# Performance work log

Hardware: AMD Instinct MI355X
Metric: run time of the kernel (lower is better)

Reference implementation:

```python
import math
import jax, jax.numpy as jnp
import numpy as np

B, LQ, LK, D, DV = 16, 2048, 2048, 256, 256


def setup_inputs() -> dict:
    key = jax.random.key(0)
    k1, k2, k3, k4 = jax.random.split(key, 4)
    query = jax.random.normal(k1, (B, LQ, D), dtype=jnp.float32)
    kmat = jax.random.normal(k2, (B, LK, D), dtype=jnp.float32)
    value = jax.random.normal(k3, (B, LK, DV), dtype=jnp.float32)
    # per-batch valid lengths in [1, LK] (avoid 0 => all -inf row)
    valid_len = jax.random.randint(k4, (B,), 1, LK + 1, dtype=jnp.int64)
    return {"query": query, "key": kmat, "value": value, "valid_len": valid_len}


def reference(query, key, value, valid_len):
    d = query.shape[-1]
    # [B, Lq, Lk] scaled dot-product scores
    scores = jnp.einsum("bqd,bkd->bqk", query, key) / math.sqrt(d)
    # mask positions k >= valid_len[b] (same mask broadcast over all queries,
    # matching the repeat(1, Lq).view(shape) in the original masked_softmax)
    mask = jnp.arange(key.shape[1])[None, None, :] < valid_len[:, None, None]
    scores = jnp.where(mask, scores, -jnp.inf)
    attn = jax.nn.softmax(scores, axis=-1)  # dropout rate is 0.0 => identity
    return jnp.einsum("bqk,bkv->bqv", attn, value)
```

## Files before the change

kernel.cpp:

```cpp
#include <hip/hip_runtime.h>
#include <hip/hip_bf16.h>

#define B_   16
#define LQ_  2048
#define LK_  2048
#define D_   256
#define DV_  256
#define MINF -1.0e30f

typedef __bf16 bf16x8_t __attribute__((ext_vector_type(8)));
typedef short  s16x8    __attribute__((ext_vector_type(8)));
typedef short  s16x4    __attribute__((ext_vector_type(4)));
typedef float  f32x4    __attribute__((ext_vector_type(4)));

__device__ __forceinline__ unsigned short f2bf(float f) {
  unsigned int u = __builtin_bit_cast(unsigned int, f);
  u += 0x7fffu + ((u >> 16) & 1u);
  return (unsigned short)(u >> 16);
}

__device__ __forceinline__ s16x8 pack8(float4 a, float4 b) {
  s16x8 r;
  r[0] = (short)f2bf(a.x); r[1] = (short)f2bf(a.y);
  r[2] = (short)f2bf(a.z); r[3] = (short)f2bf(a.w);
  r[4] = (short)f2bf(b.x); r[5] = (short)f2bf(b.y);
  r[6] = (short)f2bf(b.z); r[7] = (short)f2bf(b.w);
  return r;
}

__device__ __forceinline__ void glds16(const unsigned short* g, unsigned short* l) {
  __builtin_amdgcn_global_load_lds(
      (const __attribute__((address_space(1))) unsigned int*)g,
      (__attribute__((address_space(3))) unsigned int*)l, 16, 0, 0);
}

__global__ __launch_bounds__(256) void prep_k(const float* __restrict__ K,
                                              unsigned short* __restrict__ wsK) {
  int gid = blockIdx.x * 256 + threadIdx.x;
  int gr = gid >> 5;
  int c  = gid & 31;
  const float* src = K + ((size_t)gr << 8) + c * 8;
  float4 a = *(const float4*)(src);
  float4 b = *(const float4*)(src + 4);
  *(s16x8*)(wsK + ((size_t)gr << 8) + ((c ^ (gr & 7)) << 3)) = pack8(a, b);
}

__global__ __launch_bounds__(256) void prep_v(const float* __restrict__ V,
                                              unsigned short* __restrict__ wsV) {
  __shared__ unsigned short t[256 * 72];
  const int tid = threadIdx.x;
  const float* src = V + (size_t)blockIdx.x * 64 * 256;
  #pragma unroll
  for (int i = 0; i < 16; ++i) {
    int idx = i * 256 + tid;
    int k   = idx >> 6;
    int dv0 = (idx & 63) * 4;
    float4 x = *(const float4*)(src + k * 256 + dv0);
    t[(dv0 + 0) * 72 + k] = f2bf(x.x);
    t[(dv0 + 1) * 72 + k] = f2bf(x.y);
    t[(dv0 + 2) * 72 + k] = f2bf(x.z);
    t[(dv0 + 3) * 72 + k] = f2bf(x.w);
  }
  __syncthreads();
  unsigned short* dst = wsV + (size_t)blockIdx.x * 16384;
  #pragma unroll
  for (int i = 0; i < 8; ++i) {
    int idx = i * 256 + tid;
    int dv = idx >> 3;
    int ch = idx & 7;
    s16x8 v = *(const s16x8*)(&t[dv * 72 + ch * 8]);
    *(s16x8*)(dst + dv * 64 + ((ch ^ (dv & 7)) << 3)) = v;
  }
}

__global__ __launch_bounds__(512, 2) void attn_fwd5(
    const float* __restrict__ Q, const unsigned short* __restrict__ wsK,
    const unsigned short* __restrict__ wsV, const int* __restrict__ VL,
    float* __restrict__ O) {
  __shared__ __align__(16) unsigned short lds_all[75776];

  const int tid  = threadIdx.x;
  const int wid  = tid >> 6;
  const int lane = tid & 63;
  const int l15  = lane & 15;
  const int lg   = lane >> 4;
  const int rq   = wid & 3;
  const int kh   = wid >> 2;

  const int bid = blockIdx.x;
  const int xcd = bid & 7;
  const int j   = bid >> 3;
  const int b   = xcd + ((j >> 4) << 3);
  const int qt  = j & 15;

  int n_k = (VL[1] == 0) ? VL[2 * b] : VL[b];
  if (n_k < 1) n_k = 1;
  if (n_k > LK_) n_k = LK_;
  const int nt = (n_k + 63) >> 6;

  const int qbase = qt * 128 + rq * 32;

  s16x8 qf[2][8];
  #pragma unroll
  for (int qc = 0; qc < 2; ++qc) {
    const float* qp = Q + ((size_t)b * LQ_ + qbase + qc * 16 + l15) * D_ + lg * 8;
    #pragma unroll
    for (int dk = 0; dk < 8; ++dk) {
      float4 a = *(const float4*)(qp + dk * 32);
      float4 c = *(const float4*)(qp + dk * 32 + 4);
      qf[qc][dk] = pack8(a, c);
    }
  }

  f32x4 o[2][16];
  #pragma unroll
  for (int qc = 0; qc < 2; ++qc)
    #pragma unroll
    for (int c = 0; c < 16; ++c) o[qc][c] = (f32x4){0.f, 0.f, 0.f, 0.f};
  float m[2] = {MINF, MINF}, l[2] = {0.f, 0.f};

  const unsigned short* kbw = wsK + (size_t)b * LK_ * D_;
  const unsigned short* vbw = wsV + (size_t)b * LK_ * DV_;
  unsigned short* pw = &lds_all[65536 + wid * 1280];

#define STAGE(buf, t) do {                                                    \
    const unsigned short* ks_ = kbw + (size_t)(t) * 16384;                    \
    const unsigned short* vs_ = vbw + (size_t)(t) * 16384;                    \
    _Pragma("unroll")                                                         \
    for (int p = 0; p < 4; ++p) {                                             \
      int cu = p * 512 + wid * 64;                                            \
      glds16(ks_ + (size_t)(cu + lane) * 8, &lds_all[(buf) * 16384 + cu * 8]);\
      glds16(vs_ + (size_t)(cu + lane) * 8,                                   \
             &lds_all[32768 + (buf) * 16384 + cu * 8]);                       \
    }                                                                         \
  } while (0)

  STAGE(0, 0);

  for (int t = 0; t < nt; ++t) {
    const int cur = t & 1;
    if (t + 1 < nt) {
      STAGE(cur ^ 1, t + 1);
      asm volatile("s_waitcnt vmcnt(8)" ::: "memory");
    } else {
      asm volatile("s_waitcnt vmcnt(0)" ::: "memory");
    }
    __builtin_amdgcn_s_barrier();
    __builtin_amdgcn_sched_barrier(0);

    const unsigned short* kl = &lds_all[cur * 16384];
    f32x4 s[2][2];
    __builtin_amdgcn_s_setprio(1);
    #pragma unroll
    for (int kc = 0; kc < 2; ++kc) {
      int krow = kh * 32 + kc * 16 + l15;
      int sw = (krow & 7) << 3;
      const unsigned short* base = kl + krow * 256;
      f32x4 a0 = (f32x4){0.f, 0.f, 0.f, 0.f};
      f32x4 a1 = (f32x4){0.f, 0.f, 0.f, 0.f};
      #pragma unroll
      for (int dk = 0; dk < 8; ++dk) {
        s16x8 kf = *(const s16x8*)(base + ((dk * 32 + lg * 8) ^ sw));
        a0 = __builtin_amdgcn_mfma_f32_16x16x32_bf16(
            __builtin_bit_cast(bf16x8_t, kf),
            __builtin_bit_cast(bf16x8_t, qf[0][dk]), a0, 0, 0, 0);
        a1 = __builtin_amdgcn_mfma_f32_16x16x32_bf16(
            __builtin_bit_cast(bf16x8_t, kf),
            __builtin_bit_cast(bf16x8_t, qf[1][dk]), a1, 0, 0, 0);
      }
      s[kc][0] = a0;
      s[kc][1] = a1;
    }
    __builtin_amdgcn_s_setprio(0);

    #pragma unroll
    for (int kc = 0; kc < 2; ++kc) {
      int gk = t * 64 + kh * 32 + kc * 16 + lg * 4;
      #pragma unroll
      for (int qc = 0; qc < 2; ++qc)
        #pragma unroll
        for (int j2 = 0; j2 < 4; ++j2)
          s[kc][qc][j2] = (gk + j2 < n_k) ? s[kc][qc][j2] * 0.0625f : MINF;
    }

    float pm[2];
    #pragma unroll
    for (int qc = 0; qc < 2; ++qc) {
      float v = fmaxf(fmaxf(s[0][qc][0], s[0][qc][1]),
                      fmaxf(s[0][qc][2], s[0][qc][3]));
      v = fmaxf(v, fmaxf(fmaxf(s[1][qc][0], s[1][qc][1]),
                         fmaxf(s[1][qc][2], s[1][qc][3])));
      v = fmaxf(v, __shfl_xor(v, 16, 64));
      v = fmaxf(v, __shfl_xor(v, 32, 64));
      pm[qc] = v;
    }
    if (__any((pm[0] > m[0] + 8.0f) || (pm[1] > m[1] + 8.0f))) {
      #pragma unroll
      for (int qc = 0; qc < 2; ++qc) {
        float mn = fmaxf(m[qc], pm[qc]);
        float sc = __expf(m[qc] - mn);
        m[qc] = mn; l[qc] *= sc;
        #pragma unroll
        for (int c = 0; c < 16; ++c) o[qc][c] = o[qc][c] * sc;
      }
    }
    #pragma unroll
    for (int qc = 0; qc < 2; ++qc) {
      float p[2][4];
      #pragma unroll
      for (int kc = 0; kc < 2; ++kc)
        #pragma unroll
        for (int j2 = 0; j2 < 4; ++j2)
          p[kc][j2] = __expf(s[kc][qc][j2] - m[qc]);
      float ps = ((p[0][0] + p[0][1]) + (p[0][2] + p[0][3]))
               + ((p[1][0] + p[1][1]) + (p[1][2] + p[1][3]));
      ps += __shfl_xor(ps, 16, 64);
      ps += __shfl_xor(ps, 32, 64);
      l[qc] += ps;
      #pragma unroll
      for (int kc = 0; kc < 2; ++kc) {
        s16x4 w;
        w[0] = (short)f2bf(p[kc][0]); w[1] = (short)f2bf(p[kc][1]);
        w[2] = (short)f2bf(p[kc][2]); w[3] = (short)f2bf(p[kc][3]);
        *(s16x4*)(pw + (qc * 16 + l15) * 40 + kc * 16 + lg * 4) = w;
      }
    }

    s16x8 pb[2];
    #pragma unroll
    for (int qc = 0; qc < 2; ++qc)
      pb[qc] = *(const s16x8*)(pw + (qc * 16 + l15) * 40 + lg * 8);

    const unsigned short* vl_ = &lds_all[32768 + cur * 16384];
    __builtin_amdgcn_s_setprio(1);
    #pragma unroll
    for (int c = 0; c < 16; ++c) {
      int dv = c * 16 + l15;
      s16x8 vf = *(const s16x8*)(vl_ + dv * 64 + (((kh * 4 + lg) ^ (dv & 7)) << 3));
      o[0][c] = __builtin_amdgcn_mfma_f32_16x16x32_bf16(
          __builtin_bit_cast(bf16x8_t, vf),
          __builtin_bit_cast(bf16x8_t, pb[0]), o[0][c], 0, 0, 0);
      o[1][c] = __builtin_amdgcn_mfma_f32_16x16x32_bf16(
          __builtin_bit_cast(bf16x8_t, vf),
          __builtin_bit_cast(bf16x8_t, pb[1]), o[1][c], 0, 0, 0);
    }
    __builtin_amdgcn_s_setprio(0);

    __builtin_amdgcn_sched_barrier(0);
    __builtin_amdgcn_s_barrier();
  }

  float* mo = (float*)lds_all + rq * 8448;
  if (kh == 1) {
    #pragma unroll
    for (int qc = 0; qc < 2; ++qc) {
      #pragma unroll
      for (int c = 0; c < 16; ++c)
        *(f32x4*)(mo + (qc * 16 + l15) * 260 + c * 16 + lg * 4) = o[qc][c];
      mo[8320 + qc * 16 + l15] = m[qc];
      mo[8352 + qc * 16 + l15] = l[qc];
    }
  }
  __syncthreads();
  if (kh == 0) {
    #pragma unroll
    for (int qc = 0; qc < 2; ++qc) {
      float mb = mo[8320 + qc * 16 + l15];
      float lb = mo[8352 + qc * 16 + l15];
      float M  = fmaxf(m[qc], mb);
      float sa = __expf(m[qc] - M), sb = __expf(mb - M);
      float invL = 1.0f / (sa * l[qc] + sb * lb);
      float* ob = O + ((size_t)b * LQ_ + qbase + qc * 16 + l15) * DV_;
      #pragma unroll
      for (int c = 0; c < 16; ++c) {
        int dvb = c * 16 + lg * 4;
        f32x4 mr = *(const f32x4*)(mo + (qc * 16 + l15) * 260 + dvb);
        f32x4 r;
        #pragma unroll
        for (int j2 = 0; j2 < 4; ++j2)
          r[j2] = (sa * o[qc][c][j2] + sb * mr[j2]) * invL;
        *(f32x4*)(ob + dvb) = r;
      }
    }
  }
#undef STAGE
}

__global__ __launch_bounds__(256) void attn_fwd(
    const float* __restrict__ Q, const float* __restrict__ K,
    const float* __restrict__ V, const int* __restrict__ VL,
    float* __restrict__ O) {
  __shared__ __align__(16) unsigned short lds_k[64 * D_];
  __shared__ __align__(16) unsigned short lds_v[DV_ * 64];
  __shared__ __align__(16) unsigned short lds_p[4][16 * 64];

  const int tid  = threadIdx.x;
  const int wid  = tid >> 6;
  const int lane = tid & 63;
  const int l15  = lane & 15;
  const int lg   = lane >> 4;
  const int bid = blockIdx.x;
  const int b   = bid >> 5;
  const int qt  = bid & 31;

  int n_k = (VL[1] == 0) ? VL[2 * b] : VL[b];
  if (n_k < 1) n_k = 1;
  if (n_k > LK_) n_k = LK_;

  const int qbase = qt * 64 + wid * 16;
  s16x8 qf[8];
  {
    const float* qp = Q + ((size_t)b * LQ_ + qbase + l15) * D_ + lg * 8;
    #pragma unroll
    for (int dk = 0; dk < 8; ++dk) {
      float4 a = *(const float4*)(qp + dk * 32);
      float4 c = *(const float4*)(qp + dk * 32 + 4);
      qf[dk] = pack8(a, c);
    }
  }
  f32x4 o[16];
  #pragma unroll
  for (int c = 0; c < 16; ++c) o[c] = (f32x4){0.f, 0.f, 0.f, 0.f};
  float m[4]    = {-INFINITY, -INFINITY, -INFINITY, -INFINITY};
  float lsum[4] = {0.f, 0.f, 0.f, 0.f};
  const float* kb = K + (size_t)b * LK_ * D_;
  const float* vb = V + (size_t)b * LK_ * DV_;
  const int nt = (n_k + 63) / 64;

  for (int kt = 0; kt < nt; ++kt) {
    __syncthreads();
    {
      const float* src = kb + (size_t)kt * 64 * D_;
      #pragma unroll
      for (int p = 0; p < 8; ++p) {
        int e = (p * 256 + tid) * 8;
        int r = e >> 8;
        int d = e & 255;
        float4 a = *(const float4*)(src + e);
        float4 c = *(const float4*)(src + e + 4);
        *(s16x8*)(&lds_k[r * 256 + (d ^ ((r & 7) << 3))]) = pack8(a, c);
      }
    }
    {
      const float* src = vb + (size_t)kt * 64 * DV_;
      #pragma unroll
      for (int p = 0; p < 2; ++p) {
        int item = p * 256 + tid;
        int k0  = (item >> 5) * 4;
        int dv0 = (item & 31) * 8;
        float va[4][8];
        #pragma unroll
        for (int r = 0; r < 4; ++r) {
          float4 x = *(const float4*)(src + (k0 + r) * DV_ + dv0);
          float4 y = *(const float4*)(src + (k0 + r) * DV_ + dv0 + 4);
          va[r][0]=x.x; va[r][1]=x.y; va[r][2]=x.z; va[r][3]=x.w;
          va[r][4]=y.x; va[r][5]=y.y; va[r][6]=y.z; va[r][7]=y.w;
        }
        #pragma unroll
        for (int i = 0; i < 8; ++i) {
          int dv = dv0 + i;
          s16x4 w;
          w[0]=(short)f2bf(va[0][i]); w[1]=(short)f2bf(va[1][i]);
          w[2]=(short)f2bf(va[2][i]); w[3]=(short)f2bf(va[3][i]);
          *(s16x4*)(&lds_v[dv * 64 + (k0 ^ ((dv & 7) << 3))]) = w;
        }
      }
    }
    __syncthreads();

    f32x4 s[4];
    #pragma unroll
    for (int kc = 0; kc < 4; ++kc) {
      f32x4 acc = (f32x4){0.f, 0.f, 0.f, 0.f};
      int krow = kc * 16 + l15;
      int sw = (krow & 7) << 3;
      #pragma unroll
      for (int dk = 0; dk < 8; ++dk) {
        s16x8 kf = *(const s16x8*)(&lds_k[krow * 256 + ((dk * 32 + lg * 8) ^ sw)]);
        acc = __builtin_amdgcn_mfma_f32_16x16x32_bf16(
            __builtin_bit_cast(bf16x8_t, qf[dk]),
            __builtin_bit_cast(bf16x8_t, kf), acc, 0, 0, 0);
      }
      s[kc] = acc;
    }
    #pragma unroll
    for (int kc = 0; kc < 4; ++kc) {
      int gk = kt * 64 + kc * 16 + l15;
      #pragma unroll
      for (int j = 0; j < 4; ++j) {
        float v = s[kc][j] * 0.0625f;
        s[kc][j] = (gk < n_k) ? v : -INFINITY;
      }
    }
    float pm[4];
    #pragma unroll
    for (int j = 0; j < 4; ++j)
      pm[j] = fmaxf(fmaxf(s[0][j], s[1][j]), fmaxf(s[2][j], s[3][j]));
    #pragma unroll
    for (int off = 1; off < 16; off <<= 1) {
      #pragma unroll
      for (int j = 0; j < 4; ++j)
        pm[j] = fmaxf(pm[j], __shfl_xor(pm[j], off, 64));
    }
    float sc[4];
    #pragma unroll
    for (int j = 0; j < 4; ++j) {
      float mn = fmaxf(m[j], pm[j]);
      sc[j] = __expf(m[j] - mn);
      m[j] = mn;
    }
    float psum[4] = {0.f, 0.f, 0.f, 0.f};
    #pragma unroll
    for (int kc = 0; kc < 4; ++kc) {
      #pragma unroll
      for (int j = 0; j < 4; ++j) {
        float p = __expf(s[kc][j] - m[j]);
        psum[j] += p;
        int r = lg * 4 + j;
        lds_p[wid][r * 64 + ((kc * 16 + l15) ^ ((r & 7) << 3))] = f2bf(p);
      }
    }
    #pragma unroll
    for (int off = 1; off < 16; off <<= 1) {
      #pragma unroll
      for (int j = 0; j < 4; ++j)
        psum[j] += __shfl_xor(psum[j], off, 64);
    }
    #pragma unroll
    for (int j = 0; j < 4; ++j) lsum[j] = lsum[j] * sc[j] + psum[j];
    #pragma unroll
    for (int c = 0; c < 16; ++c) {
      #pragma unroll
      for (int j = 0; j < 4; ++j) o[c][j] *= sc[j];
    }
    s16x8 pa[2];
    #pragma unroll
    for (int kk = 0; kk < 2; ++kk)
      pa[kk] = *(const s16x8*)(&lds_p[wid][l15 * 64 + ((kk * 32 + lg * 8) ^ ((l15 & 7) << 3))]);
    #pragma unroll
    for (int c = 0; c < 16; ++c) {
      #pragma unroll
      for (int kk = 0; kk < 2; ++kk) {
        int dv = c * 16 + l15;
        s16x8 vf = *(const s16x8*)(&lds_v[dv * 64 + ((kk * 32 + lg * 8) ^ ((dv & 7) << 3))]);
        o[c] = __builtin_amdgcn_mfma_f32_16x16x32_bf16(
            __builtin_bit_cast(bf16x8_t, pa[kk]),
            __builtin_bit_cast(bf16x8_t, vf), o[c], 0, 0, 0);
      }
    }
  }
  float inv[4];
  #pragma unroll
  for (int j = 0; j < 4; ++j) inv[j] = 1.0f / lsum[j];
  float* ob = O + ((size_t)b * LQ_ + qbase) * DV_;
  #pragma unroll
  for (int c = 0; c < 16; ++c) {
    #pragma unroll
    for (int j = 0; j < 4; ++j) {
      int r = lg * 4 + j;
      ob[(size_t)r * DV_ + c * 16 + l15] = o[c][j] * inv[j];
    }
  }
}

extern "C" void kernel_launch(void* const* d_in, const int* in_sizes, int n_in,
                              void* d_out, int out_size, void* d_ws, size_t ws_size,
                              hipStream_t stream) {
  const float* Q  = (const float*)d_in[0];
  const float* K  = (const float*)d_in[1];
  const float* V  = (const float*)d_in[2];
  const int*   VL = (const int*)d_in[3];
  float* O = (float*)d_out;

  const size_t kv_elems = (size_t)B_ * LK_ * D_;
  const size_t need = kv_elems * 2 * sizeof(unsigned short);
  if (ws_size >= need) {
    unsigned short* wsK = (unsigned short*)d_ws;
    unsigned short* wsV = wsK + kv_elems;
    prep_k<<<dim3(4096), dim3(256), 0, stream>>>(K, wsK);
    prep_v<<<dim3(512), dim3(256), 0, stream>>>(V, wsV);
    attn_fwd5<<<dim3(256), dim3(512), 0, stream>>>(Q, wsK, wsV, VL, O);
  } else {
    attn_fwd<<<dim3(512), dim3(256), 0, stream>>>(Q, K, V, VL, O);
  }
}
```

Before: 142.4 us.

## Balance variable-length attention work with sorted per-block schedule of paired tiles

Adds a scheduling kernel that sorts batches by valid length and gives each of 256 persistent blocks two 64-query tiles, one from a long batch and one from a short batch, so per-block work evens out. The attention kernel drops to 256 threads with 4 waves per tile and loops over its two assigned tiles. It also defers the cross-lane row-sum reduction to the end of the loop and only shuffles the max when a rescale is needed. The trade-offs are an extra tiny launch, lower per-CU occupancy, and a serial dependency between the two tiles in each block.

```diff
diff --git a/kernel.cpp b/kernel.cpp
--- a/kernel.cpp
+++ b/kernel.cpp
@@ -73,213 +73,249 @@
   }
 }
 
-__global__ __launch_bounds__(512, 2) void attn_fwd5(
+__global__ __launch_bounds__(256) void prep_sched(const int* __restrict__ VL,
+                                                  int* __restrict__ sched) {
+  __shared__ int ord[16];
+  if (threadIdx.x == 0) {
+    int nk[16], o[16];
+    const int wide = (VL[1] == 0);
+    for (int i = 0; i < 16; ++i) {
+      int v = wide ? VL[2 * i] : VL[i];
+      if (v < 1) v = 1;
+      if (v > LK_) v = LK_;
+      nk[i] = v; o[i] = i;
+    }
+    for (int i = 1; i < 16; ++i) {
+      int key = o[i], kv = nk[key], j = i - 1;
+      while (j >= 0 && nk[o[j]] < kv) { o[j + 1] = o[j]; --j; }
+      o[j + 1] = key;
+    }
+    for (int i = 0; i < 16; ++i) ord[i] = o[i];
+  }
+  __syncthreads();
+  for (int s = threadIdx.x; s < 512; s += 256) {
+    int w  = s & 255;
+    int un = s >> 8;
+    int i  = un ? (511 - w) : w;
+    int bsel = ord[i >> 5];
+    int qt   = i & 31;
+    sched[s] = bsel | (qt << 8);
+  }
+}
+
+__global__ __launch_bounds__(256, 1) void attn_fwd10(
     const float* __restrict__ Q, const unsigned short* __restrict__ wsK,
     const unsigned short* __restrict__ wsV, const int* __restrict__ VL,
-    float* __restrict__ O) {
-  __shared__ __align__(16) unsigned short lds_all[75776];
+    const int* __restrict__ sched, float* __restrict__ O) {
+  __shared__ __align__(16) unsigned short lds_all[70144];
 
   const int tid  = threadIdx.x;
   const int wid  = tid >> 6;
   const int lane = tid & 63;
   const int l15  = lane & 15;
   const int lg   = lane >> 4;
-  const int rq   = wid & 3;
-  const int kh   = wid >> 2;
-
-  const int bid = blockIdx.x;
-  const int xcd = bid & 7;
-  const int j   = bid >> 3;
-  const int b   = xcd + ((j >> 4) << 3);
-  const int qt  = j & 15;
-
-  int n_k = (VL[1] == 0) ? VL[2 * b] : VL[b];
-  if (n_k < 1) n_k = 1;
-  if (n_k > LK_) n_k = LK_;
-  const int nt = (n_k + 63) >> 6;
-
-  const int qbase = qt * 128 + rq * 32;
-
-  s16x8 qf[2][8];
-  #pragma unroll
-  for (int qc = 0; qc < 2; ++qc) {
-    const float* qp = Q + ((size_t)b * LQ_ + qbase + qc * 16 + l15) * D_ + lg * 8;
-    #pragma unroll
-    for (int dk = 0; dk < 8; ++dk) {
-      float4 a = *(const float4*)(qp + dk * 32);
-      float4 c = *(const float4*)(qp + dk * 32 + 4);
-      qf[qc][dk] = pack8(a, c);
-    }
-  }
-
-  f32x4 o[2][16];
-  #pragma unroll
-  for (int qc = 0; qc < 2; ++qc)
-    #pragma unroll
-    for (int c = 0; c < 16; ++c) o[qc][c] = (f32x4){0.f, 0.f, 0.f, 0.f};
-  float m[2] = {MINF, MINF}, l[2] = {0.f, 0.f};
-
-  const unsigned short* kbw = wsK + (size_t)b * LK_ * D_;
-  const unsigned short* vbw = wsV + (size_t)b * LK_ * DV_;
-  unsigned short* pw = &lds_all[65536 + wid * 1280];
+  const int rq   = wid & 1;
+  const int kh   = wid >> 1;
+
+  unsigned short* pw = &lds_all[65536 + wid * 1152];
 
 #define STAGE(buf, t) do {                                                    \
     const unsigned short* ks_ = kbw + (size_t)(t) * 16384;                    \
     const unsigned short* vs_ = vbw + (size_t)(t) * 16384;                    \
     _Pragma("unroll")                                                         \
-    for (int p = 0; p < 4; ++p) {                                             \
-      int cu = p * 512 + wid * 64;                                            \
+    for (int p = 0; p < 8; ++p) {                                             \
+      int cu = p * 256 + wid * 64;                                            \
       glds16(ks_ + (size_t)(cu + lane) * 8, &lds_all[(buf) * 16384 + cu * 8]);\
       glds16(vs_ + (size_t)(cu + lane) * 8,                                   \
              &lds_all[32768 + (buf) * 16384 + cu * 8]);                       \
     }                                                                         \
   } while (0)
 
-  STAGE(0, 0);
-
-  for (int t = 0; t < nt; ++t) {
-    const int cur = t & 1;
-    if (t + 1 < nt) {
-      STAGE(cur ^ 1, t + 1);
-      asm volatile("s_waitcnt vmcnt(8)" ::: "memory");
-    } else {
-      asm volatile("s_waitcnt vmcnt(0)" ::: "memory");
-    }
-    __builtin_amdgcn_s_barrier();
-    __builtin_amdgcn_sched_barrier(0);
-
-    const unsigned short* kl = &lds_all[cur * 16384];
-    f32x4 s[2][2];
-    __builtin_amdgcn_s_setprio(1);
-    #pragma unroll
-    for (int kc = 0; kc < 2; ++kc) {
-      int krow = kh * 32 + kc * 16 + l15;
-      int sw = (krow & 7) << 3;
-      const unsigned short* base = kl + krow * 256;
-      f32x4 a0 = (f32x4){0.f, 0.f, 0.f, 0.f};
-      f32x4 a1 = (f32x4){0.f, 0.f, 0.f, 0.f};
+  for (int un = 0; un < 2; ++un) {
+    const int e  = sched[blockIdx.x + un * 256];
+    const int b  = e & 255;
+    const int qt = e >> 8;
+
+    int n_k = (VL[1] == 0) ? VL[2 * b] : VL[b];
+    if (n_k < 1) n_k = 1;
+    if (n_k > LK_) n_k = LK_;
+    const int nt = (n_k + 63) >> 6;
+
+    const int qbase = qt * 64 + rq * 32;
+
+    s16x8 qf[2][8];
+    #pragma unroll
+    for (int qc = 0; qc < 2; ++qc) {
+      const float* qp = Q + ((size_t)b * LQ_ + qbase + qc * 16 + l15) * D_ + lg * 8;
       #pragma unroll
       for (int dk = 0; dk < 8; ++dk) {
-        s16x8 kf = *(const s16x8*)(base + ((dk * 32 + lg * 8) ^ sw));
-        a0 = __builtin_amdgcn_mfma_f32_16x16x32_bf16(
-            __builtin_bit_cast(bf16x8_t, kf),
-            __builtin_bit_cast(bf16x8_t, qf[0][dk]), a0, 0, 0, 0);
-        a1 = __builtin_amdgcn_mfma_f32_16x16x32_bf16(
-            __builtin_bit_cast(bf16x8_t, kf),
-            __builtin_bit_cast(bf16x8_t, qf[1][dk]), a1, 0, 0, 0);
-      }
-      s[kc][0] = a0;
-      s[kc][1] = a1;
-    }
-    __builtin_amdgcn_s_setprio(0);
-
-    #pragma unroll
-    for (int kc = 0; kc < 2; ++kc) {
-      int gk = t * 64 + kh * 32 + kc * 16 + lg * 4;
+        float4 a = *(const float4*)(qp + dk * 32);
+        float4 c = *(const float4*)(qp + dk * 32 + 4);
+        qf[qc][dk] = pack8(a, c);
+      }
+    }
+
+    f32x4 o[2][16];
+    #pragma unroll
+    for (int qc = 0; qc < 2; ++qc)
+      #pragma unroll
+      for (int c = 0; c < 16; ++c) o[qc][c] = (f32x4){0.f, 0.f, 0.f, 0.f};
+    float m[2] = {MINF, MINF}, l[2] = {0.f, 0.f};
+
+    const unsigned short* kbw = wsK + (size_t)b * LK_ * D_;
+    const unsigned short* vbw = wsV + (size_t)b * LK_ * DV_;
+
+    __syncthreads();
+    STAGE(0, 0);
+
+    for (int t = 0; t < nt; ++t) {
+      const int cur = t & 1;
+      if (t + 1 < nt) {
+        STAGE(cur ^ 1, t + 1);
+        asm volatile("s_waitcnt vmcnt(16)" ::: "memory");
+      } else {
+        asm volatile("s_waitcnt vmcnt(0)" ::: "memory");
+      }
+      __builtin_amdgcn_s_barrier();
+      __builtin_amdgcn_sched_barrier(0);
+
+      const unsigned short* kl = &lds_all[cur * 16384];
+      f32x4 s[2][2];
+      __builtin_amdgcn_s_setprio(1);
+      #pragma unroll
+      for (int kc = 0; kc < 2; ++kc) {
+        int krow = kh * 32 + kc * 16 + l15;
+        int sw = (krow & 7) << 3;
+        const unsigned short* kbase = kl + krow * 256;
+        f32x4 a0 = (f32x4){0.f, 0.f, 0.f, 0.f};
+        f32x4 a1 = (f32x4){0.f, 0.f, 0.f, 0.f};
+        #pragma unroll
+        for (int dk = 0; dk < 8; ++dk) {
+          s16x8 kf = *(const s16x8*)(kbase + ((dk * 32 + lg * 8) ^ sw));
+          a0 = __builtin_amdgcn_mfma_f32_16x16x32_bf16(
+              __builtin_bit_cast(bf16x8_t, kf),
+              __builtin_bit_cast(bf16x8_t, qf[0][dk]), a0, 0, 0, 0);
+          a1 = __builtin_amdgcn_mfma_f32_16x16x32_bf16(
+              __builtin_bit_cast(bf16x8_t, kf),
+              __builtin_bit_cast(bf16x8_t, qf[1][dk]), a1, 0, 0, 0);
+        }
+        s[kc][0] = a0;
+        s[kc][1] = a1;
+      }
+      __builtin_amdgcn_s_setprio(0);
+
+      #pragma unroll
+      for (int kc = 0; kc < 2; ++kc) {
+        int gk = t * 64 + kh * 32 + kc * 16 + lg * 4;
+        #pragma unroll
+        for (int qc = 0; qc < 2; ++qc)
+          #pragma unroll
+          for (int j2 = 0; j2 < 4; ++j2)
+            s[kc][qc][j2] = (gk + j2 < n_k) ? s[kc][qc][j2] * 0.0625f : MINF;
+      }
+
+      float pml[2];
+      #pragma unroll
+      for (int qc = 0; qc < 2; ++qc) {
+        float v = fmaxf(fmaxf(s[0][qc][0], s[0][qc][1]),
+                        fmaxf(s[0][qc][2], s[0][qc][3]));
+        v = fmaxf(v, fmaxf(fmaxf(s[1][qc][0], s[1][qc][1]),
+                           fmaxf(s[1][qc][2], s[1][qc][3])));
+        pml[qc] = v;
+      }
+      if (__any((pml[0] > m[0] + 8.0f) || (pml[1] > m[1] + 8.0f))) {
+        #pragma unroll
+        for (int qc = 0; qc < 2; ++qc) {
+          float pm = fmaxf(pml[qc], __shfl_xor(pml[qc], 16, 64));
+          pm = fmaxf(pm, __shfl_xor(pm, 32, 64));
+          float mn = fmaxf(m[qc], pm);
+          float sc = __expf(m[qc] - mn);
+          m[qc] = mn; l[qc] *= sc;
+          #pragma unroll
+          for (int c = 0; c < 16; ++c) o[qc][c] = o[qc][c] * sc;
+        }
+      }
+      #pragma unroll
+      for (int qc = 0; qc < 2; ++qc) {
+        float p[2][4];
+        #pragma unroll
+        for (int kc = 0; kc < 2; ++kc)
+          #pragma unroll
+          for (int j2 = 0; j2 < 4; ++j2)
+            p[kc][j2] = __expf(s[kc][qc][j2] - m[qc]);
+        l[qc] += ((p[0][0] + p[0][1]) + (p[0][2] + p[0][3]))
+               + ((p[1][0] + p[1][1]) + (p[1][2] + p[1][3]));
+        #pragma unroll
+        for (int kc = 0; kc < 2; ++kc) {
+          s16x4 w;
+          w[0] = (short)f2bf(p[kc][0]); w[1] = (short)f2bf(p[kc][1]);
+          w[2] = (short)f2bf(p[kc][2]); w[3] = (short)f2bf(p[kc][3]);
+          *(s16x4*)(pw + (qc * 16 + l15) * 36 + kc * 16 + lg * 4) = w;
+        }
+      }
+
+      s16x8 pb[2];
       #pragma unroll
       for (int qc = 0; qc < 2; ++qc)
-        #pragma unroll
-        for (int j2 = 0; j2 < 4; ++j2)
-          s[kc][qc][j2] = (gk + j2 < n_k) ? s[kc][qc][j2] * 0.0625f : MINF;
-    }
-
-    float pm[2];
+        pb[qc] = *(const s16x8*)(pw + (qc * 16 + l15) * 36 + lg * 8);
+
+      const unsigned short* vl_ = &lds_all[32768 + cur * 16384];
+      __builtin_amdgcn_s_setprio(1);
+      #pragma unroll
+      for (int c = 0; c < 16; ++c) {
+        int dv = c * 16 + l15;
+        s16x8 vf = *(const s16x8*)(vl_ + dv * 64 + (((kh * 4 + lg) ^ (dv & 7)) << 3));
+        o[0][c] = __builtin_amdgcn_mfma_f32_16x16x32_bf16(
+            __builtin_bit_cast(bf16x8_t, vf),
+            __builtin_bit_cast(bf16x8_t, pb[0]), o[0][c], 0, 0, 0);
+        o[1][c] = __builtin_amdgcn_mfma_f32_16x16x32_bf16(
+            __builtin_bit_cast(bf16x8_t, vf),
+            __builtin_bit_cast(bf16x8_t, pb[1]), o[1][c], 0, 0, 0);
+      }
+      __builtin_amdgcn_s_setprio(0);
+
+      __builtin_amdgcn_sched_barrier(0);
+      __builtin_amdgcn_s_barrier();
+    }
+
     #pragma unroll
     for (int qc = 0; qc < 2; ++qc) {
-      float v = fmaxf(fmaxf(s[0][qc][0], s[0][qc][1]),
-                      fmaxf(s[0][qc][2], s[0][qc][3]));
-      v = fmaxf(v, fmaxf(fmaxf(s[1][qc][0], s[1][qc][1]),
-                         fmaxf(s[1][qc][2], s[1][qc][3])));
-      v = fmaxf(v, __shfl_xor(v, 16, 64));
-      v = fmaxf(v, __shfl_xor(v, 32, 64));
-      pm[qc] = v;
-    }
-    if (__any((pm[0] > m[0] + 8.0f) || (pm[1] > m[1] + 8.0f))) {
+      l[qc] += __shfl_xor(l[qc], 16, 64);
+      l[qc] += __shfl_xor(l[qc], 32, 64);
+    }
+
+    __syncthreads();
+    float* mo = (float*)lds_all + rq * 8448;
+    if (kh == 1) {
       #pragma unroll
       for (int qc = 0; qc < 2; ++qc) {
-        float mn = fmaxf(m[qc], pm[qc]);
-        float sc = __expf(m[qc] - mn);
-        m[qc] = mn; l[qc] *= sc;
-        #pragma unroll
-        for (int c = 0; c < 16; ++c) o[qc][c] = o[qc][c] * sc;
-      }
-    }
-    #pragma unroll
-    for (int qc = 0; qc < 2; ++qc) {
-      float p[2][4];
-      #pragma unroll
-      for (int kc = 0; kc < 2; ++kc)
-        #pragma unroll
-        for (int j2 = 0; j2 < 4; ++j2)
-          p[kc][j2] = __expf(s[kc][qc][j2] - m[qc]);
-      float ps = ((p[0][0] + p[0][1]) + (p[0][2] + p[0][3]))
-               + ((p[1][0] + p[1][1]) + (p[1][2] + p[1][3]));
-      ps += __shfl_xor(ps, 16, 64);
-      ps += __shfl_xor(ps, 32, 64);
-      l[qc] += ps;
-      #pragma unroll
-      for (int kc = 0; kc < 2; ++kc) {
-        s16x4 w;
-        w[0] = (short)f2bf(p[kc][0]); w[1] = (short)f2bf(p[kc][1]);
-        w[2] = (short)f2bf(p[kc][2]); w[3] = (short)f2bf(p[kc][3]);
-        *(s16x4*)(pw + (qc * 16 + l15) * 40 + kc * 16 + lg * 4) = w;
-      }
-    }
-
-    s16x8 pb[2];
-    #pragma unroll
-    for (int qc = 0; qc < 2; ++qc)
-      pb[qc] = *(const s16x8*)(pw + (qc * 16 + l15) * 40 + lg * 8);
-
-    const unsigned short* vl_ = &lds_all[32768 + cur * 16384];
-    __builtin_amdgcn_s_setprio(1);
-    #pragma unroll
-    for (int c = 0; c < 16; ++c) {
-      int dv = c * 16 + l15;
-      s16x8 vf = *(const s16x8*)(vl_ + dv * 64 + (((kh * 4 + lg) ^ (dv & 7)) << 3));
-      o[0][c] = __builtin_amdgcn_mfma_f32_16x16x32_bf16(
-          __builtin_bit_cast(bf16x8_t, vf),
-          __builtin_bit_cast(bf16x8_t, pb[0]), o[0][c], 0, 0, 0);
-      o[1][c] = __builtin_amdgcn_mfma_f32_16x16x32_bf16(
-          __builtin_bit_cast(bf16x8_t, vf),
-          __builtin_bit_cast(bf16x8_t, pb[1]), o[1][c], 0, 0, 0);
-    }
-    __builtin_amdgcn_s_setprio(0);
-
-    __builtin_amdgcn_sched_barrier(0);
-    __builtin_amdgcn_s_barrier();
-  }
-
-  float* mo = (float*)lds_all + rq * 8448;
-  if (kh == 1) {
-    #pragma unroll
-    for (int qc = 0; qc < 2; ++qc) {
-      #pragma unroll
-      for (int c = 0; c < 16; ++c)
-        *(f32x4*)(mo + (qc * 16 + l15) * 260 + c * 16 + lg * 4) = o[qc][c];
-      mo[8320 + qc * 16 + l15] = m[qc];
-      mo[8352 + qc * 16 + l15] = l[qc];
-    }
-  }
-  __syncthreads();
-  if (kh == 0) {
-    #pragma unroll
-    for (int qc = 0; qc < 2; ++qc) {
-      float mb = mo[8320 + qc * 16 + l15];
-      float lb = mo[8352 + qc * 16 + l15];
-      float M  = fmaxf(m[qc], mb);
-      float sa = __expf(m[qc] - M), sb = __expf(mb - M);
-      float invL = 1.0f / (sa * l[qc] + sb * lb);
-      float* ob = O + ((size_t)b * LQ_ + qbase + qc * 16 + l15) * DV_;
-      #pragma unroll
-      for (int c = 0; c < 16; ++c) {
-        int dvb = c * 16 + lg * 4;
-        f32x4 mr = *(const f32x4*)(mo + (qc * 16 + l15) * 260 + dvb);
-        f32x4 r;
-        #pragma unroll
-        for (int j2 = 0; j2 < 4; ++j2)
-          r[j2] = (sa * o[qc][c][j2] + sb * mr[j2]) * invL;
-        *(f32x4*)(ob + dvb) = r;
+        #pragma unroll
+        for (int c = 0; c < 16; ++c)
+          *(f32x4*)(mo + (qc * 16 + l15) * 260 + c * 16 + lg * 4) = o[qc][c];
+        mo[8320 + qc * 16 + l15] = m[qc];
+        mo[8352 + qc * 16 + l15] = l[qc];
+      }
+    }
+    __syncthreads();
+    if (kh == 0) {
+      #pragma unroll
+      for (int qc = 0; qc < 2; ++qc) {
+        float mb = mo[8320 + qc * 16 + l15];
+        float lb = mo[8352 + qc * 16 + l15];
+        float M  = fmaxf(m[qc], mb);
+        float sa = __expf(m[qc] - M), sb = __expf(mb - M);
+        float invL = 1.0f / (sa * l[qc] + sb * lb);
+        float* ob = O + ((size_t)b * LQ_ + qbase + qc * 16 + l15) * DV_;
+        #pragma unroll
+        for (int c = 0; c < 16; ++c) {
+          int dvb = c * 16 + lg * 4;
+          f32x4 mr = *(const f32x4*)(mo + (qc * 16 + l15) * 260 + dvb);
+          f32x4 r;
+          #pragma unroll
+          for (int j2 = 0; j2 < 4; ++j2)
+            r[j2] = (sa * o[qc][c][j2] + sb * mr[j2]) * invL;
+          *(f32x4*)(ob + dvb) = r;
+        }
       }
     }
   }
@@ -416,8 +452,8 @@
       for (int j = 0; j < 4; ++j) {
         float p = __expf(s[kc][j] - m[j]);
         psum[j] += p;
-        int r = lg * 4 + j;
-        lds_p[wid][r * 64 + ((kc * 16 + l15) ^ ((r & 7) << 3))] = f2bf(p);
+        int r2 = lg * 4 + j;
+        lds_p[wid][r2 * 64 + ((kc * 16 + l15) ^ ((r2 & 7) << 3))] = f2bf(p);
       }
     }
     #pragma unroll
@@ -457,8 +493,8 @@
   for (int c = 0; c < 16; ++c) {
     #pragma unroll
     for (int j = 0; j < 4; ++j) {
-      int r = lg * 4 + j;
-      ob[(size_t)r * DV_ + c * 16 + l15] = o[c][j] * inv[j];
+      int r2 = lg * 4 + j;
+      ob[(size_t)r2 * DV_ + c * 16 + l15] = o[c][j] * inv[j];
     }
   }
 }
@@ -473,13 +509,15 @@
   float* O = (float*)d_out;
 
   const size_t kv_elems = (size_t)B_ * LK_ * D_;
-  const size_t need = kv_elems * 2 * sizeof(unsigned short);
+  const size_t need = kv_elems * 2 * sizeof(unsigned short) + 2048;
   if (ws_size >= need) {
     unsigned short* wsK = (unsigned short*)d_ws;
     unsigned short* wsV = wsK + kv_elems;
+    int* sched = (int*)(wsV + kv_elems);
+    prep_sched<<<dim3(1), dim3(256), 0, stream>>>(VL, sched);
     prep_k<<<dim3(4096), dim3(256), 0, stream>>>(K, wsK);
     prep_v<<<dim3(512), dim3(256), 0, stream>>>(V, wsV);
-    attn_fwd5<<<dim3(256), dim3(512), 0, stream>>>(Q, wsK, wsV, VL, O);
+    attn_fwd10<<<dim3(256), dim3(256), 0, stream>>>(Q, wsK, wsV, VL, sched, O);
   } else {
     attn_fwd<<<dim3(512), dim3(256), 0, stream>>>(Q, K, V, VL, O);
   }
```

Result: no change. 139.9 us (-1.8%).
